# Performance work log

Hardware: AMD Instinct MI355X
Metric: run time of the kernel (lower is better)

The kernel has to match this reference:

```python
import jax, jax.numpy as jnp
import numpy as np

B, D_IN, C, P = 8192, 2048, 1000, 256


def setup_inputs() -> dict:
    key = jax.random.key(0)
    ks = jax.random.split(key, 6)
    return {
        "x": jax.random.normal(ks[0], (B, D_IN), dtype=jnp.float32),
        "Wm": jax.random.normal(ks[1], (C, D_IN), dtype=jnp.float32) * (1.0 / np.sqrt(D_IN)),
        "bm": jax.random.normal(ks[2], (C,), dtype=jnp.float32) * 0.01,
        "u": jax.random.normal(ks[3], (P, C), dtype=jnp.float32),
        "v": jax.random.normal(ks[4], (P, C), dtype=jnp.float32),
        "w": jax.random.normal(ks[5], (P, 1), dtype=jnp.float32),
    }


def reference(x, Wm, bm, u, v, w):
    # Backbone: Linear(D_IN -> C) producing per-instance logits (B, C)
    preds = jnp.einsum("bd,cd->bc", x, Wm) + bm
    # Gated attention, fully batched (replaces per-instance Python loop):
    # tanh(u @ pred) * sigmoid(v @ pred)  -> (B, P)
    gated = jnp.tanh(jnp.einsum("bc,pc->bp", preds, u)) * jax.nn.sigmoid(
        jnp.einsum("bc,pc->bp", preds, v)
    )
    scores = (gated @ w).ravel()          # (B,)
    attention = jax.nn.softmax(scores)    # softmax over instances
    total_pred = jnp.sum(preds * attention[:, None])
    return preds, total_pred
```

## Files before the change

### kernel.cpp

```cpp
#include <hip/hip_runtime.h>
#include <hip/hip_fp16.h>

typedef _Float16 half8 __attribute__((ext_vector_type(8)));
typedef float f32x4 __attribute__((ext_vector_type(4)));

#define B_   8192
#define DIN  2048
#define C_   1000
#define CP   1024
#define NP2  512

static const size_t OFF_XH  = 0;
static const size_t OFF_WH  = OFF_XH  + (size_t)B_ * DIN * 2;
static const size_t OFF_UVH = OFF_WH  + (size_t)CP * DIN * 2;
static const size_t OFF_PH  = OFF_UVH + (size_t)NP2 * CP * 2;
static const size_t OFF_SC  = OFF_PH  + (size_t)B_ * CP * 2;
static const size_t OFF_RS  = OFF_SC  + (size_t)B_ * 4;
static const size_t WS_NEED = OFF_RS  + (size_t)B_ * 4;

__device__ __forceinline__ void gload16(const void* g, void* l) {
  __builtin_amdgcn_global_load_lds(
      (const __attribute__((address_space(1))) void*)g,
      (__attribute__((address_space(3))) void*)l, 16, 0, 0);
}

__global__ __launch_bounds__(256) void prep_kernel(
    const float* __restrict__ x, const float* __restrict__ Wm,
    const float* __restrict__ u, const float* __restrict__ v,
    _Float16* __restrict__ xh, _Float16* __restrict__ wh,
    _Float16* __restrict__ uvh, float* __restrict__ scores,
    float* __restrict__ rowsum)
{
  const long NX  = (long)B_ * DIN / 8;
  const long NW  = (long)CP * DIN / 8;
  const long NUV = (long)NP2 * CP / 8;
  const long NZ  = 2 * (long)B_ / 8;
  const long T   = NX + NW + NUV + NZ;
  for (long idx = (long)blockIdx.x * blockDim.x + threadIdx.x; idx < T;
       idx += (long)gridDim.x * blockDim.x) {
    if (idx < NX) {
      long e = idx * 8;
      float4 p0 = *(const float4*)(x + e);
      float4 p1 = *(const float4*)(x + e + 4);
      half8 h;
      h[0] = (_Float16)p0.x; h[1] = (_Float16)p0.y; h[2] = (_Float16)p0.z; h[3] = (_Float16)p0.w;
      h[4] = (_Float16)p1.x; h[5] = (_Float16)p1.y; h[6] = (_Float16)p1.z; h[7] = (_Float16)p1.w;
      *(half8*)(xh + e) = h;
    } else if (idx < NX + NW) {
      long e = (idx - NX) * 8;
      int row = (int)(e >> 11);
      half8 h;
      if (row < C_) {
        float4 p0 = *(const float4*)(Wm + e);
        float4 p1 = *(const float4*)(Wm + e + 4);
        h[0] = (_Float16)p0.x; h[1] = (_Float16)p0.y; h[2] = (_Float16)p0.z; h[3] = (_Float16)p0.w;
        h[4] = (_Float16)p1.x; h[5] = (_Float16)p1.y; h[6] = (_Float16)p1.z; h[7] = (_Float16)p1.w;
      } else {
        h = (half8)(_Float16)0.f;
      }
      *(half8*)(wh + e) = h;
    } else if (idx < NX + NW + NUV) {
      long e = (idx - NX - NW) * 8;
      int j = (int)(e >> 10);
      int k = (int)(e & 1023);
      const float* src = (j & 1) ? v : u;
      int p = j >> 1;
      half8 h;
      #pragma unroll
      for (int t = 0; t < 8; ++t) {
        int kk = k + t;
        h[t] = (kk < C_) ? (_Float16)src[(size_t)p * C_ + kk] : (_Float16)0.f;
      }
      *(half8*)(uvh + e) = h;
    } else {
      long e = (idx - NX - NW - NUV) * 8;
      float4 z = {0.f, 0.f, 0.f, 0.f};
      if (e < B_) {
        *(float4*)(scores + e) = z; *(float4*)(scores + e + 4) = z;
      } else {
        long r = e - B_;
        *(float4*)(rowsum + r) = z; *(float4*)(rowsum + r + 4) = z;
      }
    }
  }
}

__global__ __launch_bounds__(256) void gemm1_kernel(
    const _Float16* __restrict__ xh, const _Float16* __restrict__ wh,
    const float* __restrict__ bmv, float* __restrict__ preds,
    _Float16* __restrict__ predsh, float* __restrict__ rowsum)
{
  __shared__ _Float16 sA[2][128 * 64];
  __shared__ _Float16 sB[2][128 * 64];
  const int tid  = threadIdx.x;
  const int lane = tid & 63;
  const int w    = tid >> 6;
  const int wm   = w >> 1, wn = w & 1;
  const int bm0  = blockIdx.x * 128;
  const int bn0  = blockIdx.y * 128;

  f32x4 acc[4][4] = {};

  const _Float16* srcA[4]; const _Float16* srcB[4];
  #pragma unroll
  for (int i = 0; i < 4; ++i) {
    int slot = i * 256 + tid;
    int row  = slot >> 3;
    int cb   = (slot & 7) << 4;
    int scb  = cb ^ ((row & 7) << 4);
    srcA[i] = xh + (size_t)(bm0 + row) * DIN + (scb >> 1);
    srcB[i] = wh + (size_t)(bn0 + row) * DIN + (scb >> 1);
  }
  int aoff[4][2], boff[4][2];
  #pragma unroll
  for (int mi = 0; mi < 4; ++mi) {
    #pragma unroll
    for (int ks = 0; ks < 2; ++ks) {
      int kb = ks * 64 + (lane >> 4) * 16;
      int ra = wm * 64 + mi * 16 + (lane & 15);
      aoff[mi][ks] = ra * 128 + (kb ^ ((ra & 7) << 4));
      int rb = wn * 64 + mi * 16 + (lane & 15);
      boff[mi][ks] = rb * 128 + (kb ^ ((rb & 7) << 4));
    }
  }

  auto stage = [&](int c) {
    #pragma unroll
    for (int i = 0; i < 4; ++i) {
      gload16(srcA[i], &sA[c][(i * 4 + w) * 512]);
      gload16(srcB[i], &sB[c][(i * 4 + w) * 512]);
      srcA[i] += 64; srcB[i] += 64;
    }
  };

  auto compute = [&](int c) {
    const char* bA = (const char*)&sA[c][0];
    const char* bB = (const char*)&sB[c][0];
    #pragma unroll
    for (int ks = 0; ks < 2; ++ks) {
      half8 a[4], b[4];
      #pragma unroll
      for (int mi = 0; mi < 4; ++mi) a[mi] = *(const half8*)(bA + aoff[mi][ks]);
      #pragma unroll
      for (int ni = 0; ni < 4; ++ni) b[ni] = *(const half8*)(bB + boff[ni][ks]);
      #pragma unroll
      for (int mi = 0; mi < 4; ++mi)
        #pragma unroll
        for (int ni = 0; ni < 4; ++ni)
          acc[mi][ni] = __builtin_amdgcn_mfma_f32_16x16x32_f16(a[mi], b[ni], acc[mi][ni], 0, 0, 0);
    }
  };

  const int NT = DIN / 64;
  stage(0);
  #pragma unroll 1
  for (int kt = 0; kt < NT; kt += 2) {
    stage(1);
    asm volatile("s_waitcnt vmcnt(8)" ::: "memory");
    __builtin_amdgcn_s_barrier();
    asm volatile("" ::: "memory");
    compute(0);
    __builtin_amdgcn_s_barrier();
    asm volatile("" ::: "memory");
    if (kt + 2 < NT) {
      stage(0);
      asm volatile("s_waitcnt vmcnt(8)" ::: "memory");
    } else {
      asm volatile("s_waitcnt vmcnt(0)" ::: "memory");
    }
    __builtin_amdgcn_s_barrier();
    asm volatile("" ::: "memory");
    compute(1);
    __builtin_amdgcn_s_barrier();
    asm volatile("" ::: "memory");
  }

  float rp[4][4] = {};
  #pragma unroll
  for (int mi = 0; mi < 4; ++mi) {
    #pragma unroll
    for (int ni = 0; ni < 4; ++ni) {
      f32x4 d = acc[mi][ni];
      int gc = bn0 + wn * 64 + ni * 16 + (lane & 15);
      float bias = (gc < C_) ? bmv[gc] : 0.f;
      #pragma unroll
      for (int j = 0; j < 4; ++j) {
        int gr = bm0 + wm * 64 + mi * 16 + (lane >> 4) * 4 + j;
        float val = d[j] + bias;
        predsh[(size_t)gr * CP + gc] = (_Float16)val;
        if (gc < C_) preds[(size_t)gr * C_ + gc] = val;
        rp[mi][j] += val;
      }
    }
  }
  #pragma unroll
  for (int mi = 0; mi < 4; ++mi) {
    #pragma unroll
    for (int j = 0; j < 4; ++j) {
      float s = rp[mi][j];
      s += __shfl_xor(s, 1); s += __shfl_xor(s, 2);
      s += __shfl_xor(s, 4); s += __shfl_xor(s, 8);
      if ((lane & 15) == 0) {
        int gr = bm0 + wm * 64 + mi * 16 + (lane >> 4) * 4 + j;
        atomicAdd(&rowsum[gr], s);
      }
    }
  }
}

__global__ __launch_bounds__(256) void gemm2_kernel(
    const _Float16* __restrict__ predsh, const _Float16* __restrict__ uvh,
    const float* __restrict__ wv, float* __restrict__ scores)
{
  __shared__ _Float16 sA[2][64 * 64];
  __shared__ _Float16 sB[2][128 * 64];
  const int tid  = threadIdx.x;
  const int lane = tid & 63;
  const int w    = tid >> 6;
  const int wm   = w >> 1, wn = w & 1;
  const int bm0  = blockIdx.x * 64;
  const int bn0  = blockIdx.y * 128;

  f32x4 acc[2][4] = {};

  const _Float16* srcA[2]; const _Float16* srcB[4];
  #pragma unroll
  for (int i = 0; i < 2; ++i) {
    int slot = i * 256 + tid;
    int row  = slot >> 3;
    int cb   = (slot & 7) << 4;
    int scb  = cb ^ ((row & 7) << 4);
    srcA[i] = predsh + (size_t)(bm0 + row) * CP + (scb >> 1);
  }
  #pragma unroll
  for (int i = 0; i < 4; ++i) {
    int slot = i * 256 + tid;
    int row  = slot >> 3;
    int cb   = (slot & 7) << 4;
    int scb  = cb ^ ((row & 7) << 4);
    srcB[i] = uvh + (size_t)(bn0 + row) * CP + (scb >> 1);
  }
  int aoff[2][2], boff[4][2];
  #pragma unroll
  for (int ks = 0; ks < 2; ++ks) {
    int kb = ks * 64 + (lane >> 4) * 16;
    #pragma unroll
    for (int mi = 0; mi < 2; ++mi) {
      int ra = wm * 32 + mi * 16 + (lane & 15);
      aoff[mi][ks] = ra * 128 + (kb ^ ((ra & 7) << 4));
    }
    #pragma unroll
    for (int ni = 0; ni < 4; ++ni) {
      int rb = wn * 64 + ni * 16 + (lane & 15);
      boff[ni][ks] = rb * 128 + (kb ^ ((rb & 7) << 4));
    }
  }

  auto stage = [&](int c) {
    #pragma unroll
    for (int i = 0; i < 2; ++i) {
      gload16(srcA[i], &sA[c][(i * 4 + w) * 512]);
      srcA[i] += 64;
    }
    #pragma unroll
    for (int i = 0; i < 4; ++i) {
      gload16(srcB[i], &sB[c][(i * 4 + w) * 512]);
      srcB[i] += 64;
    }
  };

  auto compute = [&](int c) {
    const char* bA = (const char*)&sA[c][0];
    const char* bB = (const char*)&sB[c][0];
    #pragma unroll
    for (int ks = 0; ks < 2; ++ks) {
      half8 a[2], b[4];
      #pragma unroll
      for (int mi = 0; mi < 2; ++mi) a[mi] = *(const half8*)(bA + aoff[mi][ks]);
      #pragma unroll
      for (int ni = 0; ni < 4; ++ni) b[ni] = *(const half8*)(bB + boff[ni][ks]);
      #pragma unroll
      for (int mi = 0; mi < 2; ++mi)
        #pragma unroll
        for (int ni = 0; ni < 4; ++ni)
          acc[mi][ni] = __builtin_amdgcn_mfma_f32_16x16x32_f16(a[mi], b[ni], acc[mi][ni], 0, 0, 0);
    }
  };

  const int NT = CP / 64;
  stage(0);
  #pragma unroll 1
  for (int kt = 0; kt < NT; kt += 2) {
    stage(1);
    asm volatile("s_waitcnt vmcnt(6)" ::: "memory");
    __builtin_amdgcn_s_barrier();
    asm volatile("" ::: "memory");
    compute(0);
    __builtin_amdgcn_s_barrier();
    asm volatile("" ::: "memory");
    if (kt + 2 < NT) {
      stage(0);
      asm volatile("s_waitcnt vmcnt(6)" ::: "memory");
    } else {
      asm volatile("s_waitcnt vmcnt(0)" ::: "memory");
    }
    __builtin_amdgcn_s_barrier();
    asm volatile("" ::: "memory");
    compute(1);
    __builtin_amdgcn_s_barrier();
    asm volatile("" ::: "memory");
  }

  float sp[2][4] = {};
  #pragma unroll
  for (int mi = 0; mi < 2; ++mi) {
    #pragma unroll
    for (int ni = 0; ni < 4; ++ni) {
      f32x4 d = acc[mi][ni];
      int gc = bn0 + wn * 64 + ni * 16 + (lane & 15);
      float wq = wv[gc >> 1];
      bool even = ((gc & 1) == 0);
      #pragma unroll
      for (int j = 0; j < 4; ++j) {
        float t  = d[j];
        float pr = __shfl_xor(t, 1);
        float th = 2.f / (1.f + __expf(-2.f * t)) - 1.f;
        float sg = 1.f / (1.f + __expf(-pr));
        sp[mi][j] += even ? (th * sg * wq) : 0.f;
      }
    }
  }
  #pragma unroll
  for (int mi = 0; mi < 2; ++mi) {
    #pragma unroll
    for (int j = 0; j < 4; ++j) {
      float s = sp[mi][j];
      s += __shfl_xor(s, 1); s += __shfl_xor(s, 2);
      s += __shfl_xor(s, 4); s += __shfl_xor(s, 8);
      if ((lane & 15) == 0) {
        int gr = bm0 + wm * 32 + mi * 16 + (lane >> 4) * 4 + j;
        atomicAdd(&scores[gr], s);
      }
    }
  }
}

__global__ __launch_bounds__(1024) void final_kernel(
    const float* __restrict__ scores, const float* __restrict__ rowsum,
    float* __restrict__ out)
{
  __shared__ float red[16], red2[16];
  const int t = threadIdx.x;
  const int lane = t & 63, wid = t >> 6;
  float s[8];
  float m = -3.4e38f;
  #pragma unroll
  for (int i = 0; i < 8; ++i) { s[i] = scores[t + i * 1024]; m = fmaxf(m, s[i]); }
  #pragma unroll
  for (int off = 1; off < 64; off <<= 1) m = fmaxf(m, __shfl_xor(m, off));
  if (lane == 0) red[wid] = m;
  __syncthreads();
  #pragma unroll
  for (int i = 0; i < 16; ++i) m = fmaxf(m, red[i]);
  __syncthreads();

  float se = 0.f, sr = 0.f;
  #pragma unroll
  for (int i = 0; i < 8; ++i) {
    float e = __expf(s[i] - m);
    se += e;
    sr += e * rowsum[t + i * 1024];
  }
  #pragma unroll
  for (int off = 1; off < 64; off <<= 1) { se += __shfl_xor(se, off); sr += __shfl_xor(sr, off); }
  if (lane == 0) { red[wid] = se; red2[wid] = sr; }
  __syncthreads();
  if (t == 0) {
    float tse = 0.f, tsr = 0.f;
    for (int i = 0; i < 16; ++i) { tse += red[i]; tsr += red2[i]; }
    out[0] = tsr / tse;
  }
}

extern "C" void kernel_launch(void* const* d_in, const int* in_sizes, int n_in,
                              void* d_out, int out_size, void* d_ws, size_t ws_size,
                              hipStream_t stream)
{
  const float* x   = (const float*)d_in[0];
  const float* Wm  = (const float*)d_in[1];
  const float* bmv = (const float*)d_in[2];
  const float* u   = (const float*)d_in[3];
  const float* v   = (const float*)d_in[4];
  const float* wv  = (const float*)d_in[5];
  float* out = (float*)d_out;

  if (ws_size < WS_NEED) return;

  char* ws = (char*)d_ws;
  _Float16* xh     = (_Float16*)(ws + OFF_XH);
  _Float16* wh     = (_Float16*)(ws + OFF_WH);
  _Float16* uvh    = (_Float16*)(ws + OFF_UVH);
  _Float16* predsh = (_Float16*)(ws + OFF_PH);
  float*    scores = (float*)(ws + OFF_SC);
  float*    rowsum = (float*)(ws + OFF_RS);

  prep_kernel<<<2048, 256, 0, stream>>>(x, Wm, u, v, xh, wh, uvh, scores, rowsum);
  gemm1_kernel<<<dim3(64, 8), 256, 0, stream>>>(xh, wh, bmv, out, predsh, rowsum);
  gemm2_kernel<<<dim3(128, 4), 256, 0, stream>>>(predsh, uvh, wv, scores);
  final_kernel<<<1, 1024, 0, stream>>>(scores, rowsum, out + (size_t)B_ * C_);
}
```

Before: 95.60 us.

## Fuse x fp32-to-fp16 conversion into gemm1 A-tile loading

```diff
diff --git a/kernel.cpp b/kernel.cpp
--- a/kernel.cpp
+++ b/kernel.cpp
@@ -10,8 +10,7 @@
 #define CP   1024
 #define NP2  512
 
-static const size_t OFF_XH  = 0;
-static const size_t OFF_WH  = OFF_XH  + (size_t)B_ * DIN * 2;
+static const size_t OFF_WH  = 0;
 static const size_t OFF_UVH = OFF_WH  + (size_t)CP * DIN * 2;
 static const size_t OFF_PH  = OFF_UVH + (size_t)NP2 * CP * 2;
 static const size_t OFF_SC  = OFF_PH  + (size_t)B_ * CP * 2;
@@ -25,29 +24,19 @@
 }
 
 __global__ __launch_bounds__(256) void prep_kernel(
-    const float* __restrict__ x, const float* __restrict__ Wm,
+    const float* __restrict__ Wm,
     const float* __restrict__ u, const float* __restrict__ v,
-    _Float16* __restrict__ xh, _Float16* __restrict__ wh,
-    _Float16* __restrict__ uvh, float* __restrict__ scores,
-    float* __restrict__ rowsum)
+    _Float16* __restrict__ wh, _Float16* __restrict__ uvh,
+    float* __restrict__ scores, float* __restrict__ rowsum)
 {
-  const long NX  = (long)B_ * DIN / 8;
   const long NW  = (long)CP * DIN / 8;
   const long NUV = (long)NP2 * CP / 8;
   const long NZ  = 2 * (long)B_ / 8;
-  const long T   = NX + NW + NUV + NZ;
+  const long T   = NW + NUV + NZ;
   for (long idx = (long)blockIdx.x * blockDim.x + threadIdx.x; idx < T;
        idx += (long)gridDim.x * blockDim.x) {
-    if (idx < NX) {
+    if (idx < NW) {
       long e = idx * 8;
-      float4 p0 = *(const float4*)(x + e);
-      float4 p1 = *(const float4*)(x + e + 4);
-      half8 h;
-      h[0] = (_Float16)p0.x; h[1] = (_Float16)p0.y; h[2] = (_Float16)p0.z; h[3] = (_Float16)p0.w;
-      h[4] = (_Float16)p1.x; h[5] = (_Float16)p1.y; h[6] = (_Float16)p1.z; h[7] = (_Float16)p1.w;
-      *(half8*)(xh + e) = h;
-    } else if (idx < NX + NW) {
-      long e = (idx - NX) * 8;
       int row = (int)(e >> 11);
       half8 h;
       if (row < C_) {
@@ -59,8 +48,8 @@
         h = (half8)(_Float16)0.f;
       }
       *(half8*)(wh + e) = h;
-    } else if (idx < NX + NW + NUV) {
-      long e = (idx - NX - NW) * 8;
+    } else if (idx < NW + NUV) {
+      long e = (idx - NW) * 8;
       int j = (int)(e >> 10);
       int k = (int)(e & 1023);
       const float* src = (j & 1) ? v : u;
@@ -73,7 +62,7 @@
       }
       *(half8*)(uvh + e) = h;
     } else {
-      long e = (idx - NX - NW - NUV) * 8;
+      long e = (idx - NW - NUV) * 8;
       float4 z = {0.f, 0.f, 0.f, 0.f};
       if (e < B_) {
         *(float4*)(scores + e) = z; *(float4*)(scores + e + 4) = z;
@@ -86,7 +75,7 @@
 }
 
 __global__ __launch_bounds__(256) void gemm1_kernel(
-    const _Float16* __restrict__ xh, const _Float16* __restrict__ wh,
+    const float* __restrict__ x, const _Float16* __restrict__ wh,
     const float* __restrict__ bmv, float* __restrict__ preds,
     _Float16* __restrict__ predsh, float* __restrict__ rowsum)
 {
@@ -101,14 +90,23 @@
 
   f32x4 acc[4][4] = {};
 
-  const _Float16* srcA[4]; const _Float16* srcB[4];
+  const float* srcA[4];
+  int dstAoff[4];
+  #pragma unroll
+  for (int i = 0; i < 4; ++i) {
+    int slot = i * 256 + tid;
+    int row  = slot >> 3;
+    int cb   = (slot & 7) << 4;
+    dstAoff[i] = row * 128 + (cb ^ ((row & 7) << 4));
+    srcA[i] = x + (size_t)(bm0 + row) * DIN + (slot & 7) * 8;
+  }
+  const _Float16* srcB[4];
   #pragma unroll
   for (int i = 0; i < 4; ++i) {
     int slot = i * 256 + tid;
     int row  = slot >> 3;
     int cb   = (slot & 7) << 4;
     int scb  = cb ^ ((row & 7) << 4);
-    srcA[i] = xh + (size_t)(bm0 + row) * DIN + (scb >> 1);
     srcB[i] = wh + (size_t)(bn0 + row) * DIN + (scb >> 1);
   }
   int aoff[4][2], boff[4][2];
@@ -124,15 +122,33 @@
     }
   }
 
-  auto stage = [&](int c) {
+  float4 ra[4][2];
+  auto loadA = [&]() {
     #pragma unroll
     for (int i = 0; i < 4; ++i) {
-      gload16(srcA[i], &sA[c][(i * 4 + w) * 512]);
+      ra[i][0] = *(const float4*)(srcA[i]);
+      ra[i][1] = *(const float4*)(srcA[i] + 4);
+      srcA[i] += 64;
+    }
+  };
+  auto writeA = [&](int c) {
+    #pragma unroll
+    for (int i = 0; i < 4; ++i) {
+      half8 h;
+      h[0] = (_Float16)ra[i][0].x; h[1] = (_Float16)ra[i][0].y;
+      h[2] = (_Float16)ra[i][0].z; h[3] = (_Float16)ra[i][0].w;
+      h[4] = (_Float16)ra[i][1].x; h[5] = (_Float16)ra[i][1].y;
+      h[6] = (_Float16)ra[i][1].z; h[7] = (_Float16)ra[i][1].w;
+      *(half8*)((char*)&sA[c][0] + dstAoff[i]) = h;
+    }
+  };
+  auto stageB = [&](int c) {
+    #pragma unroll
+    for (int i = 0; i < 4; ++i) {
       gload16(srcB[i], &sB[c][(i * 4 + w) * 512]);
-      srcA[i] += 64; srcB[i] += 64;
-    }
-  };
-
+      srcB[i] += 64;
+    }
+  };
   auto compute = [&](int c) {
     const char* bA = (const char*)&sA[c][0];
     const char* bB = (const char*)&sB[c][0];
@@ -152,28 +168,28 @@
   };
 
   const int NT = DIN / 64;
-  stage(0);
+
+  loadA();
+  stageB(0);
+  writeA(0);
+  asm volatile("s_waitcnt vmcnt(0) lgkmcnt(0)" ::: "memory");
+  __builtin_amdgcn_s_barrier();
+
   #pragma unroll 1
-  for (int kt = 0; kt < NT; kt += 2) {
-    stage(1);
-    asm volatile("s_waitcnt vmcnt(8)" ::: "memory");
-    __builtin_amdgcn_s_barrier();
-    asm volatile("" ::: "memory");
-    compute(0);
-    __builtin_amdgcn_s_barrier();
-    asm volatile("" ::: "memory");
-    if (kt + 2 < NT) {
-      stage(0);
-      asm volatile("s_waitcnt vmcnt(8)" ::: "memory");
-    } else {
-      asm volatile("s_waitcnt vmcnt(0)" ::: "memory");
-    }
-    __builtin_amdgcn_s_barrier();
-    asm volatile("" ::: "memory");
-    compute(1);
-    __builtin_amdgcn_s_barrier();
-    asm volatile("" ::: "memory");
-  }
+  for (int t = 0; t < NT - 1; ++t) {
+    const int c = t & 1;
+    loadA();
+    stageB(c ^ 1);
+    asm volatile("s_waitcnt vmcnt(12)" ::: "memory");
+    __builtin_amdgcn_s_barrier();
+    compute(c);
+    writeA(c ^ 1);
+    asm volatile("s_waitcnt lgkmcnt(0)" ::: "memory");
+    __builtin_amdgcn_s_barrier();
+  }
+  asm volatile("s_waitcnt vmcnt(0)" ::: "memory");
+  __builtin_amdgcn_s_barrier();
+  compute((NT - 1) & 1);
 
   float rp[4][4] = {};
   #pragma unroll
@@ -294,10 +310,8 @@
     stage(1);
     asm volatile("s_waitcnt vmcnt(6)" ::: "memory");
     __builtin_amdgcn_s_barrier();
-    asm volatile("" ::: "memory");
     compute(0);
     __builtin_amdgcn_s_barrier();
-    asm volatile("" ::: "memory");
     if (kt + 2 < NT) {
       stage(0);
       asm volatile("s_waitcnt vmcnt(6)" ::: "memory");
@@ -305,10 +319,8 @@
       asm volatile("s_waitcnt vmcnt(0)" ::: "memory");
     }
     __builtin_amdgcn_s_barrier();
-    asm volatile("" ::: "memory");
     compute(1);
     __builtin_amdgcn_s_barrier();
-    asm volatile("" ::: "memory");
   }
 
   float sp[2][4] = {};
@@ -397,15 +409,14 @@
   if (ws_size < WS_NEED) return;
 
   char* ws = (char*)d_ws;
-  _Float16* xh     = (_Float16*)(ws + OFF_XH);
   _Float16* wh     = (_Float16*)(ws + OFF_WH);
   _Float16* uvh    = (_Float16*)(ws + OFF_UVH);
   _Float16* predsh = (_Float16*)(ws + OFF_PH);
   float*    scores = (float*)(ws + OFF_SC);
   float*    rowsum = (float*)(ws + OFF_RS);
 
-  prep_kernel<<<2048, 256, 0, stream>>>(x, Wm, u, v, xh, wh, uvh, scores, rowsum);
-  gemm1_kernel<<<dim3(64, 8), 256, 0, stream>>>(xh, wh, bmv, out, predsh, rowsum);
+  prep_kernel<<<1288, 256, 0, stream>>>(Wm, u, v, wh, uvh, scores, rowsum);
+  gemm1_kernel<<<dim3(64, 8), 256, 0, stream>>>(x, wh, bmv, out, predsh, rowsum);
   gemm2_kernel<<<dim3(128, 4), 256, 0, stream>>>(predsh, uvh, wv, scores);
   final_kernel<<<1, 1024, 0, stream>>>(scores, rowsum, out + (size_t)B_ * C_);
 }
```

Measured after the change: 92.93 us. -2.8%, faster.

## Restructure gemm1 to 256x128 tiles, 8 waves, triple-buffered LDS pipeline

Applied to the files above, without the earlier changes.

```diff
diff --git a/kernel.cpp b/kernel.cpp
--- a/kernel.cpp
+++ b/kernel.cpp
@@ -85,123 +85,170 @@
   }
 }
 
-__global__ __launch_bounds__(256) void gemm1_kernel(
+__global__ __launch_bounds__(512) void gemm1_kernel(
     const _Float16* __restrict__ xh, const _Float16* __restrict__ wh,
     const float* __restrict__ bmv, float* __restrict__ preds,
     _Float16* __restrict__ predsh, float* __restrict__ rowsum)
 {
-  __shared__ _Float16 sA[2][128 * 64];
-  __shared__ _Float16 sB[2][128 * 64];
+  __shared__ _Float16 lds[3 * 24576];
   const int tid  = threadIdx.x;
   const int lane = tid & 63;
   const int w    = tid >> 6;
-  const int wm   = w >> 1, wn = w & 1;
-  const int bm0  = blockIdx.x * 128;
+  const int wm   = w >> 2;
+  const int wn   = w & 3;
+  const int bm0  = blockIdx.x * 256;
   const int bn0  = blockIdx.y * 128;
 
-  f32x4 acc[4][4] = {};
-
-  const _Float16* srcA[4]; const _Float16* srcB[4];
-  #pragma unroll
-  for (int i = 0; i < 4; ++i) {
-    int slot = i * 256 + tid;
+  f32x4 acc[8][2] = {};
+
+  const _Float16* srcA[4];
+  const _Float16* srcB[2];
+  #pragma unroll
+  for (int k = 0; k < 4; ++k) {
+    int slot = k * 512 + tid;
     int row  = slot >> 3;
     int cb   = (slot & 7) << 4;
     int scb  = cb ^ ((row & 7) << 4);
-    srcA[i] = xh + (size_t)(bm0 + row) * DIN + (scb >> 1);
-    srcB[i] = wh + (size_t)(bn0 + row) * DIN + (scb >> 1);
-  }
-  int aoff[4][2], boff[4][2];
-  #pragma unroll
-  for (int mi = 0; mi < 4; ++mi) {
+    srcA[k] = xh + (size_t)(bm0 + row) * DIN + (scb >> 1);
+  }
+  #pragma unroll
+  for (int k = 0; k < 2; ++k) {
+    int slot = k * 512 + tid;
+    int row  = slot >> 3;
+    int cb   = (slot & 7) << 4;
+    int scb  = cb ^ ((row & 7) << 4);
+    srcB[k] = wh + (size_t)(bn0 + row) * DIN + (scb >> 1);
+  }
+
+  int aoff[8][2], boff[2][2];
+  #pragma unroll
+  for (int m = 0; m < 8; ++m) {
     #pragma unroll
     for (int ks = 0; ks < 2; ++ks) {
+      int ra = wm * 128 + m * 16 + (lane & 15);
       int kb = ks * 64 + (lane >> 4) * 16;
-      int ra = wm * 64 + mi * 16 + (lane & 15);
-      aoff[mi][ks] = ra * 128 + (kb ^ ((ra & 7) << 4));
-      int rb = wn * 64 + mi * 16 + (lane & 15);
-      boff[mi][ks] = rb * 128 + (kb ^ ((rb & 7) << 4));
-    }
-  }
-
-  auto stage = [&](int c) {
-    #pragma unroll
-    for (int i = 0; i < 4; ++i) {
-      gload16(srcA[i], &sA[c][(i * 4 + w) * 512]);
-      gload16(srcB[i], &sB[c][(i * 4 + w) * 512]);
-      srcA[i] += 64; srcB[i] += 64;
-    }
+      aoff[m][ks] = ra * 128 + (kb ^ ((ra & 7) << 4));
+    }
+  }
+  #pragma unroll
+  for (int n = 0; n < 2; ++n) {
+    #pragma unroll
+    for (int ks = 0; ks < 2; ++ks) {
+      int rb = wn * 32 + n * 16 + (lane & 15);
+      int kb = ks * 64 + (lane >> 4) * 16;
+      boff[n][ks] = 32768 + rb * 128 + (kb ^ ((rb & 7) << 4));
+    }
+  }
+
+  auto stageSet = [&](int b, int which) {
+    char* base = (char*)lds + b * 49152;
+    if (which < 4) gload16(srcA[which], base + which * 8192 + w * 1024);
+    else           gload16(srcB[which - 4], base + 32768 + (which - 4) * 8192 + w * 1024);
   };
-
-  auto compute = [&](int c) {
-    const char* bA = (const char*)&sA[c][0];
-    const char* bB = (const char*)&sB[c][0];
-    #pragma unroll
-    for (int ks = 0; ks < 2; ++ks) {
-      half8 a[4], b[4];
-      #pragma unroll
-      for (int mi = 0; mi < 4; ++mi) a[mi] = *(const half8*)(bA + aoff[mi][ks]);
-      #pragma unroll
-      for (int ni = 0; ni < 4; ++ni) b[ni] = *(const half8*)(bB + boff[ni][ks]);
-      #pragma unroll
-      for (int mi = 0; mi < 4; ++mi)
+  auto advance = [&]() {
+    #pragma unroll
+    for (int k = 0; k < 4; ++k) srcA[k] += 64;
+    #pragma unroll
+    for (int k = 0; k < 2; ++k) srcB[k] += 64;
+  };
+
+  const int NT = DIN / 64;
+
+  #pragma unroll
+  for (int q = 0; q < 6; ++q) stageSet(0, q);
+  advance();
+  #pragma unroll
+  for (int q = 0; q < 6; ++q) stageSet(1, q);
+  advance();
+  asm volatile("s_waitcnt vmcnt(6)" ::: "memory");
+  __builtin_amdgcn_s_barrier();
+  asm volatile("" ::: "memory");
+
+  int c = 0;
+  #pragma unroll 1
+  for (int t = 0; t < NT; ++t) {
+    const char* bufc = (const char*)lds + c * 49152;
+    int sb = c - 1; if (sb < 0) sb = 2;
+    const bool st = (t + 2 < NT);
+
+    half8 a2[4][2], b2[2][2];
+    #pragma unroll
+    for (int m = 0; m < 4; ++m)
+      #pragma unroll
+      for (int ks = 0; ks < 2; ++ks)
+        a2[m][ks] = *(const half8*)(bufc + aoff[m][ks]);
+    #pragma unroll
+    for (int n = 0; n < 2; ++n)
+      #pragma unroll
+      for (int ks = 0; ks < 2; ++ks)
+        b2[n][ks] = *(const half8*)(bufc + boff[n][ks]);
+    if (st) { stageSet(sb, 0); stageSet(sb, 1); stageSet(sb, 2); }
+    __builtin_amdgcn_s_barrier();
+    asm volatile("" ::: "memory");
+    __builtin_amdgcn_s_setprio(1);
+    #pragma unroll
+    for (int m = 0; m < 4; ++m)
+      #pragma unroll
+      for (int n = 0; n < 2; ++n)
         #pragma unroll
-        for (int ni = 0; ni < 4; ++ni)
-          acc[mi][ni] = __builtin_amdgcn_mfma_f32_16x16x32_f16(a[mi], b[ni], acc[mi][ni], 0, 0, 0);
-    }
-  };
-
-  const int NT = DIN / 64;
-  stage(0);
-  #pragma unroll 1
-  for (int kt = 0; kt < NT; kt += 2) {
-    stage(1);
-    asm volatile("s_waitcnt vmcnt(8)" ::: "memory");
-    __builtin_amdgcn_s_barrier();
-    asm volatile("" ::: "memory");
-    compute(0);
-    __builtin_amdgcn_s_barrier();
-    asm volatile("" ::: "memory");
-    if (kt + 2 < NT) {
-      stage(0);
-      asm volatile("s_waitcnt vmcnt(8)" ::: "memory");
-    } else {
-      asm volatile("s_waitcnt vmcnt(0)" ::: "memory");
-    }
-    __builtin_amdgcn_s_barrier();
-    asm volatile("" ::: "memory");
-    compute(1);
-    __builtin_amdgcn_s_barrier();
-    asm volatile("" ::: "memory");
-  }
-
-  float rp[4][4] = {};
-  #pragma unroll
-  for (int mi = 0; mi < 4; ++mi) {
-    #pragma unroll
-    for (int ni = 0; ni < 4; ++ni) {
-      f32x4 d = acc[mi][ni];
-      int gc = bn0 + wn * 64 + ni * 16 + (lane & 15);
+        for (int ks = 0; ks < 2; ++ks)
+          acc[m][n] = __builtin_amdgcn_mfma_f32_16x16x32_f16(a2[m][ks], b2[n][ks], acc[m][n], 0, 0, 0);
+    __builtin_amdgcn_s_setprio(0);
+    __builtin_amdgcn_s_barrier();
+    asm volatile("" ::: "memory");
+
+    #pragma unroll
+    for (int m = 0; m < 4; ++m)
+      #pragma unroll
+      for (int ks = 0; ks < 2; ++ks)
+        a2[m][ks] = *(const half8*)(bufc + aoff[m + 4][ks]);
+    if (st) { stageSet(sb, 3); stageSet(sb, 4); stageSet(sb, 5); advance(); }
+    __builtin_amdgcn_s_barrier();
+    asm volatile("" ::: "memory");
+    __builtin_amdgcn_s_setprio(1);
+    #pragma unroll
+    for (int m = 0; m < 4; ++m)
+      #pragma unroll
+      for (int n = 0; n < 2; ++n)
+        #pragma unroll
+        for (int ks = 0; ks < 2; ++ks)
+          acc[m + 4][n] = __builtin_amdgcn_mfma_f32_16x16x32_f16(a2[m][ks], b2[n][ks], acc[m + 4][n], 0, 0, 0);
+    __builtin_amdgcn_s_setprio(0);
+    if (st)                 asm volatile("s_waitcnt vmcnt(6)" ::: "memory");
+    else if (t + 1 < NT)    asm volatile("s_waitcnt vmcnt(0)" ::: "memory");
+    __builtin_amdgcn_s_barrier();
+    asm volatile("" ::: "memory");
+
+    c = (c == 2) ? 0 : c + 1;
+  }
+
+  float rp[8][4] = {};
+  #pragma unroll
+  for (int m = 0; m < 8; ++m) {
+    #pragma unroll
+    for (int n = 0; n < 2; ++n) {
+      f32x4 d = acc[m][n];
+      int gc = bn0 + wn * 32 + n * 16 + (lane & 15);
       float bias = (gc < C_) ? bmv[gc] : 0.f;
       #pragma unroll
       for (int j = 0; j < 4; ++j) {
-        int gr = bm0 + wm * 64 + mi * 16 + (lane >> 4) * 4 + j;
+        int gr = bm0 + wm * 128 + m * 16 + (lane >> 4) * 4 + j;
         float val = d[j] + bias;
         predsh[(size_t)gr * CP + gc] = (_Float16)val;
         if (gc < C_) preds[(size_t)gr * C_ + gc] = val;
-        rp[mi][j] += val;
-      }
-    }
-  }
-  #pragma unroll
-  for (int mi = 0; mi < 4; ++mi) {
+        rp[m][j] += val;
+      }
+    }
+  }
+  #pragma unroll
+  for (int m = 0; m < 8; ++m) {
     #pragma unroll
     for (int j = 0; j < 4; ++j) {
-      float s = rp[mi][j];
+      float s = rp[m][j];
       s += __shfl_xor(s, 1); s += __shfl_xor(s, 2);
       s += __shfl_xor(s, 4); s += __shfl_xor(s, 8);
       if ((lane & 15) == 0) {
-        int gr = bm0 + wm * 64 + mi * 16 + (lane >> 4) * 4 + j;
+        int gr = bm0 + wm * 128 + m * 16 + (lane >> 4) * 4 + j;
         atomicAdd(&rowsum[gr], s);
       }
     }
@@ -405,7 +452,7 @@
   float*    rowsum = (float*)(ws + OFF_RS);
 
   prep_kernel<<<2048, 256, 0, stream>>>(x, Wm, u, v, xh, wh, uvh, scores, rowsum);
-  gemm1_kernel<<<dim3(64, 8), 256, 0, stream>>>(xh, wh, bmv, out, predsh, rowsum);
+  gemm1_kernel<<<dim3(32, 8), 512, 0, stream>>>(xh, wh, bmv, out, predsh, rowsum);
   gemm2_kernel<<<dim3(128, 4), 256, 0, stream>>>(predsh, uvh, wv, scores);
   final_kernel<<<1, 1024, 0, stream>>>(scores, rowsum, out + (size_t)B_ * C_);
 }
```

Measured after the change: 96.04 us. No clear change (+0.5%).
